# Optimization experiments

Hardware: AMD Instinct MI355X
Metric: run time of the kernel (lower is better)

## Reference

```python
import jax, jax.numpy as jnp
import numpy as np

DIM = 1024
L = 10
C = 1.0
SQRT_C = float(np.sqrt(C))


def _exp_map(x, v, c):
    # Poincare exp map (general form, as in the torch source)
    xn2 = jnp.sum(x * x, axis=-1, keepdims=True)
    lam = 2.0 / (1.0 - c * xn2)
    vn = jnp.sqrt(jnp.sum(v * v, axis=-1, keepdims=True))
    vn = jnp.maximum(vn, 1e-8)
    second = jnp.tanh(SQRT_C * lam * vn / 2.0) / (SQRT_C * vn) * v
    num = (1.0 - c * xn2) * second
    den = (1.0 - 2.0 * c * jnp.sum(x * second, axis=-1, keepdims=True)
           + c * c * xn2 * jnp.sum(second * second, axis=-1, keepdims=True))
    return x + num / den


def _log_map(x, y, c):
    # Poincare log map (general form, as in the torch source)
    xn2 = jnp.sum(x * x, axis=-1, keepdims=True)
    lam = 2.0 / (1.0 - c * xn2)
    yn2 = jnp.sum(y * y, axis=-1, keepdims=True)
    xy = jnp.sum(x * y, axis=-1, keepdims=True)
    tv = (-x * yn2 + y * (1.0 + c * xn2) - 2.0 * c * xy * x) / (1.0 - c * xn2)
    tn = jnp.sqrt(jnp.sum(tv * tv, axis=-1, keepdims=True))
    num = 2.0 * SQRT_C * jnp.arctanh(SQRT_C * tn)
    den = SQRT_C * lam * tn
    return num / den * tv


def _butterfly(u, params):
    # Stage l: blocks of size 2^l along the feature dim; within each block,
    # adjacent pairs are rotated by that block's (a, b) Givens-like rotation.
    # Param layout matches __init__: for layer l there are dim>>l blocks,
    # 2 params (a, b) each, laid out contiguously layer after layer.
    B = u.shape[0]
    offset = 0
    for l in range(L):
        bs = 1 << l
        nb = DIM // bs
        seg = params[offset:offset + 2 * nb]
        offset += 2 * nb
        if bs < 2:
            continue  # block of size 1 has no pair to rotate
        ab = seg.reshape(nb, 2)
        a = ab[:, 0][None, :, None]  # [1, nb, 1]
        b = ab[:, 1][None, :, None]
        u4 = u.reshape(B, nb, bs // 2, 2)
        u0 = u4[..., 0]
        u1 = u4[..., 1]
        u = jnp.stack([a * u0 + b * u1, -b * u0 + a * u1], axis=-1).reshape(B, DIM)
    return u


def setup_inputs() -> dict:
    key = jax.random.key(0)
    k1, k2 = jax.random.split(key)
    # points inside the Poincare ball: per-row norm ~ 0.01*sqrt(1024) ~ 0.32
    x = jax.random.normal(k1, (32768, DIM), dtype=jnp.float32) * 0.01
    P = 2 * sum(DIM >> l for l in range(L))  # 4092
    base = jnp.tile(jnp.array([0.9, 0.0], dtype=jnp.float32), P // 2)
    params = base + 0.1 * jax.random.normal(k2, (P,), dtype=jnp.float32)
    return {"x": x, "params": params}


def reference(x, params):
    u = _log_map(jnp.zeros_like(x), x, C)
    u = _butterfly(u, params)
    return _exp_map(jnp.zeros_like(u), u, C)
```

## Files before the change

### kernel.cpp

```cpp
#include <hip/hip_runtime.h>
#include <math.h>

#define DIM 1024
#define NPAIRS 512
#define NLEVELS 9

__global__ void butterfly_weights_kernel(const float* __restrict__ params,
                                         float2* __restrict__ w) {
    int p = blockIdx.x * blockDim.x + threadIdx.x;
    if (p >= NPAIRS) return;
    float wr = 1.0f, wi = 0.0f;
    int off = 2 * DIM;
#pragma unroll
    for (int l = 1; l <= NLEVELS; ++l) {
        int j = p >> (l - 1);
        float a = params[off + 2 * j];
        float b = params[off + 2 * j + 1];
        float nr = wr * a + wi * b;
        float ni = wi * a - wr * b;
        wr = nr;
        wi = ni;
        off += 2 * (DIM >> l);
    }
    w[p] = make_float2(wr, wi);
}

__device__ __forceinline__ float block_reduce_sum(float val, float* red) {
#pragma unroll
    for (int o = 32; o > 0; o >>= 1) val += __shfl_down(val, o);
    int lane = threadIdx.x & 63;
    int wave = threadIdx.x >> 6;
    if (lane == 0) red[wave] = val;
    __syncthreads();
    if (threadIdx.x == 0) red[4] = red[0] + red[1] + red[2] + red[3];
    __syncthreads();
    return red[4];
}

__global__ __launch_bounds__(256) void hyper_butterfly_kernel(
        const float* __restrict__ x,
        const float4* __restrict__ w4,
        float* __restrict__ out) {
    __shared__ float red0[8];
    __shared__ float red1[8];

    const int t = threadIdx.x;
    const size_t row = blockIdx.x;
    const float4* xrow = (const float4*)(x + row * (size_t)DIM);

    float4 v = xrow[t];

    float part = v.x * v.x + v.y * v.y + v.z * v.z + v.w * v.w;
    float xn2 = block_reduce_sum(part, red0);
    float r = sqrtf(xn2);
    float s1 = (r > 1e-12f) ? (0.5f * logf((1.0f + r) / (1.0f - r)) / r) : 1.0f;

    float4 u;
    u.x = s1 * v.x;
    u.y = s1 * v.y;
    u.z = s1 * v.z;
    u.w = s1 * v.w;

    float4 wv = w4[t];
    float4 y;
    y.x = wv.x * u.x - wv.y * u.y;
    y.y = wv.x * u.y + wv.y * u.x;
    y.z = wv.z * u.z - wv.w * u.w;
    y.w = wv.z * u.w + wv.w * u.z;

    float part2 = y.x * y.x + y.y * y.y + y.z * y.z + y.w * y.w;
    float un2 = block_reduce_sum(part2, red1);
    float vn = fmaxf(sqrtf(un2), 1e-8f);
    float s2 = tanhf(vn) / vn;

    float4 o;
    o.x = s2 * y.x;
    o.y = s2 * y.y;
    o.z = s2 * y.z;
    o.w = s2 * y.w;

    float4* orow = (float4*)(out + row * (size_t)DIM);
    orow[t] = o;
}

extern "C" void kernel_launch(void* const* d_in, const int* in_sizes, int n_in,
                              void* d_out, int out_size, void* d_ws, size_t ws_size,
                              hipStream_t stream) {
    const float* x = (const float*)d_in[0];
    const float* params = (const float*)d_in[1];
    float* out = (float*)d_out;
    float2* w = (float2*)d_ws;

    int rows = in_sizes[0] / DIM;

    butterfly_weights_kernel<<<1, NPAIRS, 0, stream>>>(params, w);
    hyper_butterfly_kernel<<<rows, DIM / 4, 0, stream>>>(x, (const float4*)w, out);
}
```

Measured before the change: 222.6 us.

## Fuse weight precompute into main kernel with wave-per-row persistent grid

Drops the separate weight-precompute launch. Each thread now computes its own 8 combined butterfly weights into registers, once per block. Each row is handled by a single wave with shuffle-only reductions, which removes the shared-memory block reductions and barriers. A persistent grid of 2048 blocks strides over the rows. The cost is redundant per-block weight computation, 72 scattered parameter loads per thread, and more registers.

```diff
diff --git a/kernel.cpp b/kernel.cpp
--- a/kernel.cpp
+++ b/kernel.cpp
@@ -2,85 +2,91 @@
 #include <math.h>
 
 #define DIM 1024
-#define NPAIRS 512
 #define NLEVELS 9
+#define ROWS_PER_BLOCK 4
+#define NBLOCKS 2048
 
-__global__ void butterfly_weights_kernel(const float* __restrict__ params,
-                                         float2* __restrict__ w) {
-    int p = blockIdx.x * blockDim.x + threadIdx.x;
-    if (p >= NPAIRS) return;
-    float wr = 1.0f, wi = 0.0f;
-    int off = 2 * DIM;
+__global__ __launch_bounds__(256) void hyper_butterfly_fused(
+        const float* __restrict__ x,
+        const float* __restrict__ params,
+        float* __restrict__ out,
+        int rows) {
+    const int lane = threadIdx.x & 63;
+    const int wave = threadIdx.x >> 6;
+
+    float4 W[4];
 #pragma unroll
-    for (int l = 1; l <= NLEVELS; ++l) {
-        int j = p >> (l - 1);
-        float a = params[off + 2 * j];
-        float b = params[off + 2 * j + 1];
-        float nr = wr * a + wi * b;
-        float ni = wi * a - wr * b;
-        wr = nr;
-        wi = ni;
-        off += 2 * (DIM >> l);
+    for (int k = 0; k < 4; ++k) {
+        const int base_pair = 2 * (lane + 64 * k);
+#pragma unroll
+        for (int h = 0; h < 2; ++h) {
+            const int p = base_pair + h;
+            float wr = 1.0f, wi = 0.0f;
+            int off = 2 * DIM;
+#pragma unroll
+            for (int l = 1; l <= NLEVELS; ++l) {
+                const int j = p >> (l - 1);
+                const float a = params[off + 2 * j];
+                const float b = params[off + 2 * j + 1];
+                const float nr = wr * a + wi * b;
+                const float ni = wi * a - wr * b;
+                wr = nr; wi = ni;
+                off += 2 * (DIM >> l);
+            }
+            if (h == 0) { W[k].x = wr; W[k].y = wi; }
+            else        { W[k].z = wr; W[k].w = wi; }
+        }
     }
-    w[p] = make_float2(wr, wi);
-}
 
-__device__ __forceinline__ float block_reduce_sum(float val, float* red) {
+    const int row0 = blockIdx.x * ROWS_PER_BLOCK + wave;
+    const int row_stride = gridDim.x * ROWS_PER_BLOCK;
+
+    for (int row = row0; row < rows; row += row_stride) {
+        const float4* xrow = (const float4*)(x + (size_t)row * DIM);
+        float4 v[4];
 #pragma unroll
-    for (int o = 32; o > 0; o >>= 1) val += __shfl_down(val, o);
-    int lane = threadIdx.x & 63;
-    int wave = threadIdx.x >> 6;
-    if (lane == 0) red[wave] = val;
-    __syncthreads();
-    if (threadIdx.x == 0) red[4] = red[0] + red[1] + red[2] + red[3];
-    __syncthreads();
-    return red[4];
-}
+        for (int k = 0; k < 4; ++k) v[k] = xrow[lane + 64 * k];
 
-__global__ __launch_bounds__(256) void hyper_butterfly_kernel(
-        const float* __restrict__ x,
-        const float4* __restrict__ w4,
-        float* __restrict__ out) {
-    __shared__ float red0[8];
-    __shared__ float red1[8];
+        float xn2 = 0.0f;
+#pragma unroll
+        for (int k = 0; k < 4; ++k)
+            xn2 += v[k].x * v[k].x + v[k].y * v[k].y +
+                   v[k].z * v[k].z + v[k].w * v[k].w;
+#pragma unroll
+        for (int m = 32; m > 0; m >>= 1) xn2 += __shfl_xor(xn2, m);
 
-    const int t = threadIdx.x;
-    const size_t row = blockIdx.x;
-    const float4* xrow = (const float4*)(x + row * (size_t)DIM);
+        const float r = sqrtf(xn2);
+        const float s1 = (r > 1e-12f)
+                             ? (0.5f * logf((1.0f + r) / (1.0f - r)) / r)
+                             : 1.0f;
 
-    float4 v = xrow[t];
+        float un2 = 0.0f;
+#pragma unroll
+        for (int k = 0; k < 4; ++k) {
+            const float ux = s1 * v[k].x, uy = s1 * v[k].y;
+            const float uz = s1 * v[k].z, uw = s1 * v[k].w;
+            v[k].x = W[k].x * ux - W[k].y * uy;
+            v[k].y = W[k].x * uy + W[k].y * ux;
+            v[k].z = W[k].z * uz - W[k].w * uw;
+            v[k].w = W[k].z * uw + W[k].w * uz;
+            un2 += v[k].x * v[k].x + v[k].y * v[k].y +
+                   v[k].z * v[k].z + v[k].w * v[k].w;
+        }
+#pragma unroll
+        for (int m = 32; m > 0; m >>= 1) un2 += __shfl_xor(un2, m);
 
-    float part = v.x * v.x + v.y * v.y + v.z * v.z + v.w * v.w;
-    float xn2 = block_reduce_sum(part, red0);
-    float r = sqrtf(xn2);
-    float s1 = (r > 1e-12f) ? (0.5f * logf((1.0f + r) / (1.0f - r)) / r) : 1.0f;
+        const float vn = fmaxf(sqrtf(un2), 1e-8f);
+        const float s2 = tanhf(vn) / vn;
 
-    float4 u;
-    u.x = s1 * v.x;
-    u.y = s1 * v.y;
-    u.z = s1 * v.z;
-    u.w = s1 * v.w;
-
-    float4 wv = w4[t];
-    float4 y;
-    y.x = wv.x * u.x - wv.y * u.y;
-    y.y = wv.x * u.y + wv.y * u.x;
-    y.z = wv.z * u.z - wv.w * u.w;
-    y.w = wv.z * u.w + wv.w * u.z;
-
-    float part2 = y.x * y.x + y.y * y.y + y.z * y.z + y.w * y.w;
-    float un2 = block_reduce_sum(part2, red1);
-    float vn = fmaxf(sqrtf(un2), 1e-8f);
-    float s2 = tanhf(vn) / vn;
-
-    float4 o;
-    o.x = s2 * y.x;
-    o.y = s2 * y.y;
-    o.z = s2 * y.z;
-    o.w = s2 * y.w;
-
-    float4* orow = (float4*)(out + row * (size_t)DIM);
-    orow[t] = o;
+        float4* orow = (float4*)(out + (size_t)row * DIM);
+#pragma unroll
+        for (int k = 0; k < 4; ++k) {
+            float4 o;
+            o.x = s2 * v[k].x; o.y = s2 * v[k].y;
+            o.z = s2 * v[k].z; o.w = s2 * v[k].w;
+            orow[lane + 64 * k] = o;
+        }
+    }
 }
 
 extern "C" void kernel_launch(void* const* d_in, const int* in_sizes, int n_in,
@@ -89,10 +95,11 @@
     const float* x = (const float*)d_in[0];
     const float* params = (const float*)d_in[1];
     float* out = (float*)d_out;
-    float2* w = (float2*)d_ws;
 
-    int rows = in_sizes[0] / DIM;
+    const int rows = in_sizes[0] / DIM;
+    int nblocks = NBLOCKS;
+    const int max_needed = (rows + ROWS_PER_BLOCK - 1) / ROWS_PER_BLOCK;
+    if (nblocks > max_needed) nblocks = max_needed;
 
-    butterfly_weights_kernel<<<1, NPAIRS, 0, stream>>>(params, w);
-    hyper_butterfly_kernel<<<rows, DIM / 4, 0, stream>>>(x, (const float4*)w, out);
+    hyper_butterfly_fused<<<nblocks, 256, 0, stream>>>(x, params, out, rows);
 }
```

Measured after the change: 233.7 us. 5.0% more time.
